# Performance work log

Measured on AMD Instinct MI355X. Metric: run time of the kernel, lower is better.

## Reference

```python
import jax, jax.numpy as jnp
from jax import lax
import numpy as np

LN_EPS = 1e-5

def layernorm(x, g, b):
    m = jnp.mean(x, axis=-1, keepdims=True)
    v = jnp.mean((x - m) ** 2, axis=-1, keepdims=True)
    return (x - m) / jnp.sqrt(v + LN_EPS) * g + b

def setup_inputs() -> dict:
    key = jax.random.key(0)
    ks = jax.random.split(key, 16)
    B, C, T = 64, 8, 2048
    K, L = 128, 64
    E, NC = 64, 10
    s = 0.05
    d = {}
    d["x"] = jax.random.normal(ks[0], (B, C, T), jnp.float32)
    d["shapelets"] = jax.random.uniform(ks[1], (K, C, L), jnp.float32, -1.0, 1.0)
    # local encoder: Linear(K->E) + LayerNorm
    d["w_loc"] = jax.random.normal(ks[2], (K, E), jnp.float32) * s
    d["b_loc"] = jnp.zeros((E,), jnp.float32)
    d["g_loc"] = jnp.ones((E,), jnp.float32)
    d["be_loc"] = jnp.zeros((E,), jnp.float32)
    # global conv: Conv2d(1->16,(3,5)) , Conv2d(16->32,(3,5))
    d["conv1_w"] = jax.random.normal(ks[3], (16, 1, 3, 5), jnp.float32) * s
    d["conv1_b"] = jnp.zeros((16,), jnp.float32)
    d["conv2_w"] = jax.random.normal(ks[4], (32, 16, 3, 5), jnp.float32) * s
    d["conv2_b"] = jnp.zeros((32,), jnp.float32)
    # global encoder: Linear(32->E) + LayerNorm
    d["w_glob"] = jax.random.normal(ks[5], (32, E), jnp.float32) * s
    d["b_glob"] = jnp.zeros((E,), jnp.float32)
    d["g_glob"] = jnp.ones((E,), jnp.float32)
    d["be_glob"] = jnp.zeros((E,), jnp.float32)
    # MultiheadAttention (torch layout): in_proj (3E,E), out_proj (E,E)
    d["in_proj_w"] = jax.random.normal(ks[6], (3 * E, E), jnp.float32) * s
    d["in_proj_b"] = jnp.zeros((3 * E,), jnp.float32)
    d["out_w"] = jax.random.normal(ks[7], (E, E), jnp.float32) * s
    d["out_b"] = jnp.zeros((E,), jnp.float32)
    # MLP head: Linear(E->E//2), Linear(E//2->NC)
    d["mlp_w1"] = jax.random.normal(ks[8], (E, E // 2), jnp.float32) * s
    d["mlp_b1"] = jnp.zeros((E // 2,), jnp.float32)
    d["mlp_w2"] = jax.random.normal(ks[9], (E // 2, NC), jnp.float32) * s
    d["mlp_b2"] = jnp.zeros((NC,), jnp.float32)
    return d

def reference(x, shapelets, w_loc, b_loc, g_loc, be_loc,
              conv1_w, conv1_b, conv2_w, conv2_b,
              w_glob, b_glob, g_glob, be_glob,
              in_proj_w, in_proj_b, out_w, out_b,
              mlp_w1, mlp_b1, mlp_w2, mlp_b2):
    B, C, T = x.shape
    K, _, L = shapelets.shape
    n_heads = 8
    # ---- shapelet min squared distance via ||w||^2 - 2*corr + ||s||^2 ----
    # corr: (B, K, W) with W = T - L + 1; same math as the unfold/broadcast version
    corr = lax.conv_general_dilated(x, shapelets, (1,), 'VALID',
                                    dimension_numbers=('NCH', 'OIH', 'NCH'))
    win_sq = lax.conv_general_dilated(x * x, jnp.ones((1, C, L), x.dtype), (1,), 'VALID',
                                      dimension_numbers=('NCH', 'OIH', 'NCH'))  # (B,1,W)
    s_sq = jnp.sum(shapelets * shapelets, axis=(1, 2))  # (K,)
    dist_sq = win_sq - 2.0 * corr + s_sq[None, :, None]  # (B,K,W)
    feat = jnp.min(dist_sq, axis=2)  # (B,K)
    # ---- local encoder ----
    local = layernorm(jax.nn.relu(feat @ w_loc + b_loc), g_loc, be_loc)  # (B,E)
    # ---- global conv branch on (B,1,C,T) ----
    h = x[:, None, :, :]
    h = lax.conv_general_dilated(h, conv1_w, (1, 1), [(1, 1), (2, 2)],
                                 dimension_numbers=('NCHW', 'OIHW', 'NCHW'))
    h = jax.nn.relu(h + conv1_b[None, :, None, None])
    h = lax.reduce_window(h, -jnp.inf, lax.max, (1, 1, 1, 2), (1, 1, 1, 2), 'VALID')
    h = lax.conv_general_dilated(h, conv2_w, (1, 1), [(1, 1), (2, 2)],
                                 dimension_numbers=('NCHW', 'OIHW', 'NCHW'))
    h = jax.nn.relu(h + conv2_b[None, :, None, None])
    h = lax.reduce_window(h, -jnp.inf, lax.max, (1, 1, 1, 2), (1, 1, 1, 2), 'VALID')
    g = jnp.mean(h, axis=(2, 3))  # AdaptiveAvgPool2d((1,1)) + Flatten -> (B,32)
    glob = layernorm(jax.nn.relu(g @ w_glob + b_glob), g_glob, be_glob)  # (B,E)
    # ---- cross attention (query len 1, kv len 1) ----
    E = local.shape[-1]
    hd = E // n_heads
    wq, wk, wv = jnp.split(in_proj_w, 3, axis=0)
    bq, bk, bv = jnp.split(in_proj_b, 3)
    q = (local @ wq.T + bq).reshape(B, n_heads, hd)
    k = (glob @ wk.T + bk).reshape(B, n_heads, hd)
    v = (glob @ wv.T + bv).reshape(B, n_heads, hd)
    scores = jnp.sum(q * k, axis=-1, keepdims=True) / jnp.sqrt(jnp.float32(hd))  # (B,H,1)
    attn = jax.nn.softmax(scores, axis=-1)  # kv length 1 -> all ones
    attn_out = (attn * v).reshape(B, E) @ out_w.T + out_b  # (B,E)
    # ---- MLP head (dropout is identity in eval) ----
    hmid = jax.nn.relu(attn_out @ mlp_w1 + mlp_b1)
    return hmid @ mlp_w2 + mlp_b2
```

## Files before the change

### kernel.cpp

```cpp
#include <hip/hip_runtime.h>
#include <math.h>


typedef __attribute__((ext_vector_type(8)))  _Float16 f16x8;
typedef __attribute__((ext_vector_type(16))) float    f32x16;

#define WT 64
#define NT 16
#define H1_OFF   0
#define XS_OFF   21760
#define LDS_BYTES 26368

__global__ void prep_frags(const float* __restrict__ w2, _Float16* __restrict__ fragg) {
    const int t    = blockIdx.x;
    const int lane = threadIdx.x;
    const int kh   = t / 5, kw = t - kh * 5;
    const int oc   = lane & 31;
    const int ic0  = (lane >> 5) * 8;
    f16x8 hv;
    #pragma unroll
    for (int j = 0; j < 8; ++j)
        hv[j] = (_Float16)w2[((oc * 16 + ic0 + j) * 3 + kh) * 5 + kw];
    *(f16x8*)&fragg[(t * 64 + lane) * 8] = hv;
}

__global__ __launch_bounds__(256, 4) void conv_fused(
    const float* __restrict__ x,
    const float* __restrict__ w1, const float* __restrict__ b1,
    const float* __restrict__ b2,
    const _Float16* __restrict__ fragg,
    float* __restrict__ part)
{
    const int wt  = blockIdx.x;
    const int b   = blockIdx.y;
    const int tid = threadIdx.x;
    const int w0  = wt * WT;

    __shared__ __align__(16) unsigned int ldsu[LDS_BYTES / 4];
    _Float16* h1 = (_Float16*)((char*)ldsu + H1_OFF);
    float*    xs = (float*)((char*)ldsu + XS_OFF);

    const int ic1 = tid & 15;
    const int s   = tid >> 4;
    float wreg[15];
    #pragma unroll
    for (int k = 0; k < 15; ++k) wreg[k] = w1[ic1 * 15 + k];
    const float bias1 = b1[ic1];

    const int t0 = 2 * w0 - 6;
    for (int i = tid; i < 8 * 144; i += 256) {
        int r = i / 144, tl = i - r * 144;
        int t = t0 + tl;
        float v = 0.f;
        if (tl < 140 && t >= 0 && t < 2048) v = x[(b * 8 + r) * 2048 + t];
        xs[i] = v;
    }
    {
        unsigned int* hh = (unsigned int*)h1;
        for (int i = tid; i < 544; i += 256) {
            hh[i] = 0u; hh[4896 + i] = 0u;
        }
    }
    __syncthreads();

    {
        int r = 0, c4 = s;
        while (c4 >= 17) { c4 -= 17; ++r; }
        for (int j = s; j < 136; j += 16) {
            const int cb = c4 * 8;
            float xv[3][12];
            #pragma unroll
            for (int q = 0; q < 3; ++q) {
                int rr = r + q - 1;
                if (rr >= 0 && rr < 8) {
                    const float4* p = (const float4*)&xs[rr * 144 + cb];
                    float4 a0 = p[0], a1 = p[1], a2 = p[2];
                    xv[q][0]=a0.x; xv[q][1]=a0.y; xv[q][2]=a0.z; xv[q][3]=a0.w;
                    xv[q][4]=a1.x; xv[q][5]=a1.y; xv[q][6]=a1.z; xv[q][7]=a1.w;
                    xv[q][8]=a2.x; xv[q][9]=a2.y; xv[q][10]=a2.z; xv[q][11]=a2.w;
                } else {
                    #pragma unroll
                    for (int z = 0; z < 12; ++z) xv[q][z] = 0.f;
                }
            }
            const int ib = ((r + 1) * 68 + 4 * c4) * 16 + ic1;
            #pragma unroll
            for (int cc = 0; cc < 4; ++cc) {
                float c0 = bias1, c1 = bias1;
                #pragma unroll
                for (int kh = 0; kh < 3; ++kh)
                    #pragma unroll
                    for (int kw = 0; kw < 5; ++kw) {
                        float wgt = wreg[kh * 5 + kw];
                        c0 = fmaf(xv[kh][2 * cc + kw],     wgt, c0);
                        c1 = fmaf(xv[kh][2 * cc + kw + 1], wgt, c1);
                    }
                float v = fmaxf(fmaxf(c0, c1), 0.f);
                int wc = w0 - 2 + 4 * c4 + cc;
                if (wc < 0 || wc >= 1024) v = 0.f;
                h1[ib + cc * 16] = (_Float16)v;
            }
            c4 += 16;
            if (c4 >= 17) { c4 -= 17; ++r; }
        }
    }
    __syncthreads();

    const int lane  = tid & 63;
    const int wave  = tid >> 6;
    const int laneN = lane & 31;
    const int icoff = (lane >> 5) * 8;
    const int half  = lane >> 5;

    f32x16 acc[4];
    #pragma unroll
    for (int nt = 0; nt < 4; ++nt)
        #pragma unroll
        for (int r = 0; r < 16; ++r) acc[nt][r] = 0.f;

    const f16x8* Ag = (const f16x8*)fragg;
    f16x8 a_cur = Ag[lane];
    for (int t = 0; t < 15; ++t) {
        f16x8 a_nxt = (t < 14) ? Ag[(t + 1) * 64 + lane] : a_cur;
        int kh = t / 5, kw = t - kh * 5;
        #pragma unroll
        for (int nt = 0; nt < 4; ++nt) {
            int hrow = 2 * wave + (nt >> 1);
            int wn0  = (nt & 1) * 32;
            int idx  = ((hrow + kh) * 68 + wn0 + laneN + kw) * 16 + icoff;
            f16x8 bv = *(const f16x8*)&h1[idx];
            acc[nt] = __builtin_amdgcn_mfma_f32_32x32x16_f16(a_cur, bv, acc[nt], 0, 0, 0);
        }
        a_cur = a_nxt;
    }

    float b2v[16], sums[16];
    #pragma unroll
    for (int r = 0; r < 16; ++r) {
        b2v[r]  = b2[(r & 3) + 8 * (r >> 2) + 4 * half];
        sums[r] = 0.f;
    }
    #pragma unroll
    for (int nt = 0; nt < 4; ++nt)
        #pragma unroll
        for (int r = 0; r < 16; ++r) {
            float d = acc[nt][r] + b2v[r];
            float o = fmaxf(fmaxf(d, __shfl_xor(d, 1)), 0.f);
            sums[r] += o;
        }
    #pragma unroll
    for (int r = 0; r < 16; ++r)
        #pragma unroll
        for (int k = 1; k <= 16; k <<= 1)
            sums[r] += __shfl_xor(sums[r], k);
    if (laneN == 0) {
        #pragma unroll
        for (int r = 0; r < 16; ++r) {
            int oc = (r & 3) + 8 * (r >> 2) + 4 * half;
            part[((b * 32 + oc) * 16 + wt) * 4 + wave] = 0.5f * sums[r];
        }
    }
}

__global__ void tail_kernel(
    const float* __restrict__ part,
    const float* __restrict__ w_glob, const float* __restrict__ b_glob,
    const float* __restrict__ g_glob, const float* __restrict__ be_glob,
    const float* __restrict__ in_proj_w, const float* __restrict__ in_proj_b,
    const float* __restrict__ out_w, const float* __restrict__ out_b,
    const float* __restrict__ mlp_w1, const float* __restrict__ mlp_b1,
    const float* __restrict__ mlp_w2, const float* __restrict__ mlp_b2,
    float* __restrict__ out)
{
    const int b = blockIdx.x;
    const int e = threadIdx.x;
    __shared__ float gs[32], glob_s[64], vs[64], aos[64], hms[32];

    if (e < 32) {
        float sm = 0.f;
        #pragma unroll
        for (int t = 0; t < 64; ++t) sm += part[(b * 32 + e) * 64 + t];
        gs[e] = sm * (1.f / 4096.f);
    }
    __syncthreads();

    float acc = b_glob[e];
    #pragma unroll
    for (int i = 0; i < 32; ++i) acc = fmaf(gs[i], w_glob[i * 64 + e], acc);
    acc = fmaxf(acc, 0.f);

    float m = acc;
    #pragma unroll
    for (int k = 32; k >= 1; k >>= 1) m += __shfl_xor(m, k);
    m *= (1.f / 64.f);
    float d = acc - m;
    float vv = d * d;
    #pragma unroll
    for (int k = 32; k >= 1; k >>= 1) vv += __shfl_xor(vv, k);
    vv *= (1.f / 64.f);
    float gl = d * (1.f / sqrtf(vv + 1e-5f)) * g_glob[e] + be_glob[e];
    glob_s[e] = gl;
    __syncthreads();

    float vval = in_proj_b[128 + e];
    #pragma unroll
    for (int j = 0; j < 64; ++j) vval = fmaf(glob_s[j], in_proj_w[(128 + e) * 64 + j], vval);
    vs[e] = vval;
    __syncthreads();

    float ao = out_b[e];
    #pragma unroll
    for (int j = 0; j < 64; ++j) ao = fmaf(vs[j], out_w[e * 64 + j], ao);
    aos[e] = ao;
    __syncthreads();

    if (e < 32) {
        float hm = mlp_b1[e];
        #pragma unroll
        for (int j = 0; j < 64; ++j) hm = fmaf(aos[j], mlp_w1[j * 32 + e], hm);
        hms[e] = fmaxf(hm, 0.f);
    }
    __syncthreads();

    if (e < 10) {
        float o = mlp_b2[e];
        #pragma unroll
        for (int i = 0; i < 32; ++i) o = fmaf(hms[i], mlp_w2[i * 10 + e], o);
        out[b * 10 + e] = o;
    }
}

extern "C" void kernel_launch(void* const* d_in, const int* in_sizes, int n_in,
                              void* d_out, int out_size, void* d_ws, size_t ws_size,
                              hipStream_t stream) {
    const float* x        = (const float*)d_in[0];
    const float* conv1_w  = (const float*)d_in[6];
    const float* conv1_b  = (const float*)d_in[7];
    const float* conv2_w  = (const float*)d_in[8];
    const float* conv2_b  = (const float*)d_in[9];
    const float* w_glob   = (const float*)d_in[10];
    const float* b_glob   = (const float*)d_in[11];
    const float* g_glob   = (const float*)d_in[12];
    const float* be_glob  = (const float*)d_in[13];
    const float* in_proj_w = (const float*)d_in[14];
    const float* in_proj_b = (const float*)d_in[15];
    const float* out_w    = (const float*)d_in[16];
    const float* out_b    = (const float*)d_in[17];
    const float* mlp_w1   = (const float*)d_in[18];
    const float* mlp_b1   = (const float*)d_in[19];
    const float* mlp_w2   = (const float*)d_in[20];
    const float* mlp_b2   = (const float*)d_in[21];

    _Float16* fragg = (_Float16*)d_ws;
    float* partials = (float*)((char*)d_ws + 15360);

    prep_frags<<<15, 64, 0, stream>>>(conv2_w, fragg);

    dim3 grid(NT, 64);
    conv_fused<<<grid, 256, 0, stream>>>(x, conv1_w, conv1_b, conv2_b, fragg, partials);

    tail_kernel<<<64, 64, 0, stream>>>(partials, w_glob, b_glob, g_glob, be_glob,
                                       in_proj_w, in_proj_b, out_w, out_b,
                                       mlp_w1, mlp_b1, mlp_w2, mlp_b2,
                                       (float*)d_out);
}
```

Baseline: 124.9 us.

## Remap conv1 thread work to 4 channels per thread and use DPP reductions

The conv1 stage now has each thread compute four input channels per output position. This reuses the loaded x window across channels and writes packed f16x4 values to LDS, instead of doing one channel per thread over a strided loop. The conv2 epilogue swaps shuffle-based pair max and lane reductions for DPP row operations and reduces only within 16-lane rows. This doubles the number of partial sums written to global memory, and the tail kernel now sums 128 partials instead of 64. The trade-off is more registers per thread (60 weights plus 4 biases), which may hurt occupancy, and larger partial-buffer traffic.

New measurement: 123.6 us, median of 2. About the same (-1.0%).

```diff
diff --git a/kernel.cpp b/kernel.cpp
--- a/kernel.cpp
+++ b/kernel.cpp
@@ -2,6 +2,7 @@
 #include <math.h>
 
 
+typedef __attribute__((ext_vector_type(4))) _Float16 f16x4;
 typedef __attribute__((ext_vector_type(8)))  _Float16 f16x8;
 typedef __attribute__((ext_vector_type(16))) float    f32x16;
 
@@ -10,6 +11,16 @@
 #define H1_OFF   0
 #define XS_OFF   21760
 #define LDS_BYTES 26368
+
+template <int CTRL>
+__device__ __forceinline__ float dppf(float v) {
+    return __uint_as_float(__builtin_amdgcn_update_dpp(
+        0u, __float_as_uint(v), CTRL, 0xF, 0xF, true));
+}
+#define DPP_XOR1 0xB1
+#define DPP_XOR2 0x4E
+#define DPP_ROR4 0x124
+#define DPP_ROR8 0x128
 
 __global__ void prep_frags(const float* __restrict__ w2, _Float16* __restrict__ fragg) {
     const int t    = blockIdx.x;
@@ -40,12 +51,15 @@
     _Float16* h1 = (_Float16*)((char*)ldsu + H1_OFF);
     float*    xs = (float*)((char*)ldsu + XS_OFF);
 
-    const int ic1 = tid & 15;
-    const int s   = tid >> 4;
-    float wreg[15];
-    #pragma unroll
-    for (int k = 0; k < 15; ++k) wreg[k] = w1[ic1 * 15 + k];
-    const float bias1 = b1[ic1];
+    const int q = tid & 3;
+    float wreg[60];
+    float bias1[4];
+    #pragma unroll
+    for (int j = 0; j < 4; ++j) {
+        #pragma unroll
+        for (int k = 0; k < 15; ++k) wreg[j * 15 + k] = w1[(q * 4 + j) * 15 + k];
+        bias1[j] = b1[q * 4 + j];
+    }
 
     const int t0 = 2 * w0 - 6;
     for (int i = tid; i < 8 * 144; i += 256) {
@@ -63,45 +77,48 @@
     }
     __syncthreads();
 
-    {
-        int r = 0, c4 = s;
-        while (c4 >= 17) { c4 -= 17; ++r; }
-        for (int j = s; j < 136; j += 16) {
-            const int cb = c4 * 8;
-            float xv[3][12];
+    #pragma unroll
+    for (int pass = 0; pass < 3; ++pass) {
+        if (pass == 2 && tid >= 32) break;
+        const int idx = (tid >> 2) + pass * 64;
+        const int r   = idx / 17;
+        const int c4  = idx - r * 17;
+        const int cb  = c4 * 8;
+        float xv[3][12];
+        #pragma unroll
+        for (int pq = 0; pq < 3; ++pq) {
+            int rr = r + pq - 1;
+            if (rr >= 0 && rr < 8) {
+                const float4* p = (const float4*)&xs[rr * 144 + cb];
+                float4 a0 = p[0], a1 = p[1], a2 = p[2];
+                xv[pq][0]=a0.x; xv[pq][1]=a0.y; xv[pq][2]=a0.z; xv[pq][3]=a0.w;
+                xv[pq][4]=a1.x; xv[pq][5]=a1.y; xv[pq][6]=a1.z; xv[pq][7]=a1.w;
+                xv[pq][8]=a2.x; xv[pq][9]=a2.y; xv[pq][10]=a2.z; xv[pq][11]=a2.w;
+            } else {
+                #pragma unroll
+                for (int z = 0; z < 12; ++z) xv[pq][z] = 0.f;
+            }
+        }
+        #pragma unroll
+        for (int cc = 0; cc < 4; ++cc) {
+            const int wc = w0 - 2 + 4 * c4 + cc;
+            f16x4 hv;
             #pragma unroll
-            for (int q = 0; q < 3; ++q) {
-                int rr = r + q - 1;
-                if (rr >= 0 && rr < 8) {
-                    const float4* p = (const float4*)&xs[rr * 144 + cb];
-                    float4 a0 = p[0], a1 = p[1], a2 = p[2];
-                    xv[q][0]=a0.x; xv[q][1]=a0.y; xv[q][2]=a0.z; xv[q][3]=a0.w;
-                    xv[q][4]=a1.x; xv[q][5]=a1.y; xv[q][6]=a1.z; xv[q][7]=a1.w;
-                    xv[q][8]=a2.x; xv[q][9]=a2.y; xv[q][10]=a2.z; xv[q][11]=a2.w;
-                } else {
-                    #pragma unroll
-                    for (int z = 0; z < 12; ++z) xv[q][z] = 0.f;
-                }
-            }
-            const int ib = ((r + 1) * 68 + 4 * c4) * 16 + ic1;
-            #pragma unroll
-            for (int cc = 0; cc < 4; ++cc) {
-                float c0 = bias1, c1 = bias1;
+            for (int j = 0; j < 4; ++j) {
+                float c0 = bias1[j], c1 = bias1[j];
                 #pragma unroll
                 for (int kh = 0; kh < 3; ++kh)
                     #pragma unroll
                     for (int kw = 0; kw < 5; ++kw) {
-                        float wgt = wreg[kh * 5 + kw];
+                        float wgt = wreg[j * 15 + kh * 5 + kw];
                         c0 = fmaf(xv[kh][2 * cc + kw],     wgt, c0);
                         c1 = fmaf(xv[kh][2 * cc + kw + 1], wgt, c1);
                     }
                 float v = fmaxf(fmaxf(c0, c1), 0.f);
-                int wc = w0 - 2 + 4 * c4 + cc;
                 if (wc < 0 || wc >= 1024) v = 0.f;
-                h1[ib + cc * 16] = (_Float16)v;
+                hv[j] = (_Float16)v;
             }
-            c4 += 16;
-            if (c4 >= 17) { c4 -= 17; ++r; }
+            *(f16x4*)&h1[((r + 1) * 68 + 4 * c4 + cc) * 16 + q * 4] = hv;
         }
     }
     __syncthreads();
@@ -145,19 +162,24 @@
         #pragma unroll
         for (int r = 0; r < 16; ++r) {
             float d = acc[nt][r] + b2v[r];
-            float o = fmaxf(fmaxf(d, __shfl_xor(d, 1)), 0.f);
+            float o = fmaxf(fmaxf(d, dppf<DPP_XOR1>(d)), 0.f);
             sums[r] += o;
         }
     #pragma unroll
-    for (int r = 0; r < 16; ++r)
-        #pragma unroll
-        for (int k = 1; k <= 16; k <<= 1)
-            sums[r] += __shfl_xor(sums[r], k);
-    if (laneN == 0) {
+    for (int r = 0; r < 16; ++r) {
+        float s = sums[r];
+        s += dppf<DPP_XOR1>(s);
+        s += dppf<DPP_XOR2>(s);
+        s += dppf<DPP_ROR4>(s);
+        s += dppf<DPP_ROR8>(s);
+        sums[r] = s;
+    }
+    if ((lane & 15) == 0) {
+        const int nh = (lane >> 4) & 1;
         #pragma unroll
         for (int r = 0; r < 16; ++r) {
             int oc = (r & 3) + 8 * (r >> 2) + 4 * half;
-            part[((b * 32 + oc) * 16 + wt) * 4 + wave] = 0.5f * sums[r];
+            part[((b * 32 + oc) * 16 + wt) * 8 + wave * 2 + nh] = 0.5f * sums[r];
         }
     }
 }
@@ -179,7 +201,7 @@
     if (e < 32) {
         float sm = 0.f;
         #pragma unroll
-        for (int t = 0; t < 64; ++t) sm += part[(b * 32 + e) * 64 + t];
+        for (int t = 0; t < 128; ++t) sm += part[(b * 32 + e) * 128 + t];
         gs[e] = sm * (1.f / 4096.f);
     }
     __syncthreads();
```
